# Performance work log

Measured on AMD Instinct MI355X. Metric: run time of the kernel, lower is better.

The kernel has to match this reference:

```python
import jax, jax.numpy as jnp
import numpy as np

DIM = 256
N_EMBED = 20
KL_WEIGHT = 1e-08
TAU = 1.0
EPS = 1e-10
N_RES = 3


def conv3x3(x, w, b):
    # x: [B,C,H,W], w: [O,I,3,3], b: [O]
    y = jax.lax.conv_general_dilated(
        x, w, window_strides=(1, 1), padding=((1, 1), (1, 1)),
        dimension_numbers=('NCHW', 'OIHW', 'NCHW'))
    return y + b[None, :, None, None]


def setup_inputs() -> dict:
    key = jax.random.key(0)
    ks = jax.random.split(key, 12)
    B, H, W = 8, 128, 128
    s = 1.0 / np.sqrt(DIM * 9)
    return {
        'x': jax.random.normal(ks[0], (B, DIM, H, W), dtype=jnp.float32),
        'gumbel_u': jax.random.uniform(ks[1], (B, N_EMBED, 1, 1), dtype=jnp.float32),
        'W_map': jax.random.normal(ks[2], (DIM, DIM), dtype=jnp.float32) / np.sqrt(DIM),
        'proj_w': jax.random.normal(ks[3], (N_EMBED, DIM), dtype=jnp.float32) / np.sqrt(DIM),
        'proj_b': jnp.zeros((N_EMBED,), dtype=jnp.float32),
        'embed': jax.random.normal(ks[4], (N_EMBED, DIM), dtype=jnp.float32),
        'res_w1': jax.random.normal(ks[5], (N_RES, DIM, DIM, 3, 3), dtype=jnp.float32) * s,
        'res_b1': jnp.zeros((N_RES, DIM), dtype=jnp.float32),
        'res_w2': jax.random.normal(ks[6], (N_RES, DIM, DIM, 3, 3), dtype=jnp.float32) * s,
        'res_b2': jnp.zeros((N_RES, DIM), dtype=jnp.float32),
    }


def reference(x, gumbel_u, W_map, proj_w, proj_b, embed, res_w1, res_b1, res_w2, res_b2):
    # --- mapping network: global avg pool -> 1x1 conv -> sigmoid ---
    pooled = jnp.mean(x, axis=(2, 3), keepdims=True)            # [B,C,1,1]
    m = jax.nn.sigmoid(jnp.einsum('oc,bchw->bohw', W_map, pooled))

    # --- GumbelQuantize ---
    logits = jnp.einsum('nc,bchw->bnhw', proj_w, m) + proj_b[None, :, None, None]
    g = -jnp.log(-jnp.log(gumbel_u + EPS) + EPS)                 # gumbel noise
    y_soft = jax.nn.softmax((logits + g) / TAU, axis=1)
    idx = jnp.argmax(y_soft, axis=1)                             # [B,1,1]
    y_hard = jax.nn.one_hot(idx, N_EMBED, axis=1, dtype=y_soft.dtype)
    # straight-through hard one-hot
    one_hot = y_hard + y_soft - jax.lax.stop_gradient(y_soft)
    piror = jnp.einsum('bnhw,nd->bdhw', one_hot, embed)          # [B,C,1,1]

    # KL to uniform (computed but discarded by WPGM.forward; kept for fidelity)
    qy = jax.nn.softmax(logits, axis=1)
    _diff = KL_WEIGHT * jnp.mean(jnp.sum(qy * jnp.log(qy * N_EMBED + EPS), axis=1))

    # --- residual add + 3 ResBlocks (conv3x3 -> relu -> conv3x3 + skip) ---
    h = x + piror
    for i in range(N_RES):
        h = h + conv3x3(jax.nn.relu(conv3x3(h, res_w1[i], res_b1[i])), res_w2[i], res_b2[i])
    return h
```

## Files before the change

### kernel.cpp

```cpp
#include <hip/hip_runtime.h>

typedef unsigned int uint32;
typedef __attribute__((ext_vector_type(8))) short short8;
typedef __attribute__((ext_vector_type(4))) float f32x4;

__device__ inline float bf2f(unsigned short u){ return __uint_as_float(((uint32)u)<<16); }
__device__ inline unsigned short f2bf(float f){
    uint32 x = __float_as_uint(f);
    x += 0x7fffu + ((x>>16)&1u);
    return (unsigned short)(x>>16);
}

__global__ __launch_bounds__(256) void pool_kernel(const float* __restrict__ x,
                                                   float* __restrict__ pooled){
    int bc = blockIdx.x;
    const float4* row = (const float4*)(x + (size_t)bc*16384);
    float s = 0.f;
#pragma unroll
    for(int k=0;k<16;k++){ float4 v = row[threadIdx.x + k*256]; s += v.x+v.y+v.z+v.w; }
    for(int off=32; off; off>>=1) s += __shfl_down(s, off, 64);
    __shared__ float ls[4];
    int lane = threadIdx.x & 63, w = threadIdx.x >> 6;
    if(lane==0) ls[w] = s;
    __syncthreads();
    if(threadIdx.x==0) pooled[bc] = (ls[0]+ls[1]+ls[2]+ls[3]) * (1.0f/16384.0f);
}

__global__ __launch_bounds__(256) void head_kernel(const float* __restrict__ W_map,
                                                   const float* __restrict__ proj_w,
                                                   const float* __restrict__ proj_b,
                                                   const float* __restrict__ embed,
                                                   const float* __restrict__ gu,
                                                   const float* __restrict__ pooled,
                                                   float* __restrict__ piror){
    __shared__ float m[256];
    __shared__ float lg[20];
    __shared__ int sidx;
    int t = threadIdx.x;
    for(int b=0;b<8;b++){
        float s = 0.f;
        const float* wr = W_map + (size_t)t*256;
        const float* pb = pooled + b*256;
        for(int c=0;c<256;c++) s += wr[c]*pb[c];
        m[t] = 1.0f/(1.0f+__expf(-s));
        __syncthreads();
        if(t<20){
            float s2 = 0.f;
            const float* pw = proj_w + (size_t)t*256;
            for(int c=0;c<256;c++) s2 += pw[c]*m[c];
            float u = gu[b*20+t];
            float g = -logf(-logf(u + 1e-10f) + 1e-10f);
            lg[t] = s2 + proj_b[t] + g;
        }
        __syncthreads();
        if(t==0){
            int best = 0; float bv = lg[0];
            for(int n=1;n<20;n++) if(lg[n] > bv){ bv = lg[n]; best = n; }
            sidx = best;
        }
        __syncthreads();
        piror[b*256+t] = embed[(size_t)sidx*256 + t];
        __syncthreads();
    }
}

__global__ __launch_bounds__(256) void pack_kernel(const float* __restrict__ x,
                                                   const float* __restrict__ piror,
                                                   unsigned short* __restrict__ h){
    __shared__ float tile[64][65];
    int bx = blockIdx.x;
    int b    =  bx >> 10;
    int cblk = (bx >> 8) & 3;
    int pblk =  bx & 255;
    int c0 = cblk*64, p0 = pblk*64;
    int col = threadIdx.x & 63;
    int r0  = threadIdx.x >> 6;
    const float* xb = x + ((size_t)(b*256 + c0))*16384 + p0;
#pragma unroll
    for(int it=0; it<16; it++){
        int r = r0 + it*4;
        tile[r][col] = xb[(size_t)r*16384 + col];
    }
    __syncthreads();
    float pir = piror[b*256 + c0 + col];
    unsigned short* hb = h + ((size_t)(b*16384 + p0))*256 + c0;
#pragma unroll
    for(int it=0; it<16; it++){
        int p = r0 + it*4;
        hb[(size_t)p*256 + col] = f2bf(tile[col][p] + pir);
    }
}

__global__ __launch_bounds__(256) void wtrans_kernel(const float* __restrict__ w1,
                                                     const float* __restrict__ w2,
                                                     unsigned short* __restrict__ wT){
    int bx = blockIdx.x;
    int o  = bx & 255;
    int tt = bx >> 8;
    int cv = tt / 9, tap = tt % 9;
    int res = cv >> 1;
    const float* src = ((cv & 1) ? w2 : w1) + (size_t)res * 589824;
    int c = threadIdx.x;
    float v = src[((size_t)o*256 + c)*9 + tap];
    wT[(size_t)bx*256 + c] = f2bf(v);
}

template<int MODE>
__global__ __launch_bounds__(256, 2)
void conv_kernel(const unsigned short* __restrict__ src,
                 const unsigned short* __restrict__ wTc,
                 const float* __restrict__ bias,
                 unsigned short* __restrict__ dst,
                 const unsigned short* __restrict__ hskip,
                 float* __restrict__ out,
                 const unsigned short* __restrict__ zp){
    __shared__ unsigned short ldsX[3*4160];
    __shared__ unsigned short ldsW[2][256*32];
    int tid  = threadIdx.x;
    int bid  = blockIdx.x;
    int b    = bid & 7;
    int y    = bid >> 3;
    int pt   = b*128 + y;

    int lane = tid & 63, wid = tid >> 6;
    int l15  = lane & 15, quad = lane >> 4;

    if(tid < 96){
        int r = tid >> 5, side = (tid >> 4) & 1, dw = tid & 15;
        ((int*)ldsX)[r*2080 + (side ? 129*16 : 0) + dw] = 0;
    }

    const unsigned short* xbase[6];
    int xdst[6];
#pragma unroll
    for(int t=0;t<6;t++){
        int qb = t*256 + wid*64;
        int rb = qb >> 9;
        int cb = qb & 511;
        int q  = qb + lane;
        int p  = (q & 511) >> 2;
        int k  = q & 3;
        int kk = k ^ ((p+1)&3);
        int yy = y + rb - 1;
        xbase[t] = ((unsigned)yy < 128u)
                 ? src + ((size_t)((b*128+yy)*128 + p))*256 + kk*8
                 : zp + kk*8;
        xdst[t] = rb*4160 + 32 + cb*8;
    }
    const unsigned short* wbase[4];
    int wdst[4];
#pragma unroll
    for(int t=0;t<4;t++){
        int qb = t*256 + wid*64;
        int q  = qb + lane;
        int o  = q >> 2;
        int kk = (q & 3) ^ (o & 3);
        wbase[t] = wTc + ((size_t)o)*256 + kk*8;
        wdst[t]  = qb*8;
    }
    int aoff[4];
#pragma unroll
    for(int i=0;i<4;i++){
        int o = wid*64 + i*16 + l15;
        aoff[i] = o*32 + ((quad ^ (o&3))*8);
    }

    f32x4 acc[4][8];
#pragma unroll
    for(int i=0;i<4;i++)
#pragma unroll
        for(int j=0;j<8;j++){ f32x4 z = {0.f,0.f,0.f,0.f}; acc[i][j] = z; }

    for(int cc=0; cc<8; cc++){
#pragma unroll
        for(int t=0;t<6;t++)
            __builtin_amdgcn_global_load_lds(
                (const __attribute__((address_space(1))) void*)(xbase[t] + cc*32),
                (__attribute__((address_space(3))) void*)&ldsX[xdst[t]], 16, 0, 0);
#pragma unroll
        for(int t=0;t<4;t++)
            __builtin_amdgcn_global_load_lds(
                (const __attribute__((address_space(1))) void*)(wbase[t] + cc*32),
                (__attribute__((address_space(3))) void*)&ldsW[0][wdst[t]], 16, 0, 0);
        __syncthreads();

        for(int tap=0; tap<9; tap++){
            int d = tap & 1;
            if(tap < 8){
#pragma unroll
                for(int t=0;t<4;t++)
                    __builtin_amdgcn_global_load_lds(
                        (const __attribute__((address_space(1))) void*)(wbase[t] + (size_t)(tap+1)*65536 + cc*32),
                        (__attribute__((address_space(3))) void*)&ldsW[d^1][wdst[t]], 16, 0, 0);
            }
            int rr = tap / 3;
            int dx = tap % 3 - 1;

            short8 av[4], bv[8];
#pragma unroll
            for(int i=0;i<4;i++) av[i] = *(const short8*)&ldsW[d][aoff[i]];
#pragma unroll
            for(int j=0;j<8;j++){
                int s = j*16 + l15 + dx + 1;
                bv[j] = *(const short8*)&ldsX[rr*4160 + s*32 + ((quad ^ (s&3))*8)];
            }
#pragma unroll
            for(int i=0;i<4;i++)
#pragma unroll
                for(int j=0;j<8;j++)
                    acc[i][j] = __builtin_amdgcn_mfma_f32_16x16x32_bf16(av[i], bv[j], acc[i][j], 0,0,0);
            __syncthreads();
        }
    }

    size_t gprow = (size_t)pt*128;
#pragma unroll
    for(int i=0;i<4;i++){
        int o = wid*64 + i*16 + quad*4;
        float4 bb = *(const float4*)&bias[o];
        float bias4[4] = {bb.x, bb.y, bb.z, bb.w};
#pragma unroll
        for(int j=0;j<8;j++){
            int p = j*16 + l15;
            size_t gpix = gprow + p;
            float v[4];
#pragma unroll
            for(int r=0;r<4;r++) v[r] = acc[i][j][r] + bias4[r];
            if(MODE==0){
#pragma unroll
                for(int r=0;r<4;r++) v[r] = fmaxf(v[r], 0.0f);
                ushort4 st; st.x=f2bf(v[0]); st.y=f2bf(v[1]); st.z=f2bf(v[2]); st.w=f2bf(v[3]);
                *(ushort4*)&dst[gpix*256 + o] = st;
            } else {
                ushort4 sk = *(const ushort4*)&hskip[gpix*256 + o];
                v[0]+=bf2f(sk.x); v[1]+=bf2f(sk.y); v[2]+=bf2f(sk.z); v[3]+=bf2f(sk.w);
                if(MODE==1){
                    ushort4 st; st.x=f2bf(v[0]); st.y=f2bf(v[1]); st.z=f2bf(v[2]); st.w=f2bf(v[3]);
                    *(ushort4*)&dst[gpix*256 + o] = st;
                } else {
                    size_t outbase = ((size_t)(b*256 + o))*16384 + (size_t)y*128 + p;
#pragma unroll
                    for(int r=0;r<4;r++) out[outbase + (size_t)r*16384] = v[r];
                }
            }
        }
    }
}

extern "C" void kernel_launch(void* const* d_in, const int* in_sizes, int n_in,
                              void* d_out, int out_size, void* d_ws, size_t ws_size,
                              hipStream_t stream){
    const float* x      = (const float*)d_in[0];
    const float* gu     = (const float*)d_in[1];
    const float* W_map  = (const float*)d_in[2];
    const float* proj_w = (const float*)d_in[3];
    const float* proj_b = (const float*)d_in[4];
    const float* embed  = (const float*)d_in[5];
    const float* rw1    = (const float*)d_in[6];
    const float* rb1    = (const float*)d_in[7];
    const float* rw2    = (const float*)d_in[8];
    const float* rb2    = (const float*)d_in[9];
    float* out = (float*)d_out;

    char* ws = (char*)d_ws;
    unsigned short* zp     = (unsigned short*)(ws + 0);
    float*          pooled = (float*)(ws + 4096);
    float*          piror  = (float*)(ws + 16384);
    unsigned short* wT     = (unsigned short*)(ws + 32768);
    unsigned short* hbuf   = (unsigned short*)(ws + ((size_t)8<<20));
    unsigned short* tbuf   = (unsigned short*)(ws + ((size_t)8<<20) + ((size_t)64<<20));

    hipMemsetAsync(zp, 0, 1024, stream);
    pool_kernel<<<2048, 256, 0, stream>>>(x, pooled);
    head_kernel<<<1, 256, 0, stream>>>(W_map, proj_w, proj_b, embed, gu, pooled, piror);
    pack_kernel<<<8192, 256, 0, stream>>>(x, piror, hbuf);
    wtrans_kernel<<<13824, 256, 0, stream>>>(rw1, rw2, wT);

    for(int res=0; res<3; res++){
        const unsigned short* w1c = wT + (size_t)(res*2+0)*9*65536;
        const unsigned short* w2c = wT + (size_t)(res*2+1)*9*65536;
        conv_kernel<0><<<1024, 256, 0, stream>>>(hbuf, w1c, rb1 + res*256, tbuf, nullptr, nullptr, zp);
        if(res < 2)
            conv_kernel<1><<<1024, 256, 0, stream>>>(tbuf, w2c, rb2 + res*256, hbuf, hbuf, nullptr, zp);
        else
            conv_kernel<2><<<1024, 256, 0, stream>>>(tbuf, w2c, rb2 + res*256, nullptr, hbuf, out, zp);
    }
}
```

Measured before the change: 1.241 ms.

## Load conv weights directly into registers and double-buffer input rows in LDS

Weight fragments are now read straight from global memory into registers, prefetched one tap ahead, and the LDS weight staging buffer is removed. The input-row tile becomes double-buffered, so the next channel chunk loads during compute, and the per-tap barriers are replaced by a single barrier per chunk. The LDS swizzle for the input tile changes to a pair-based XOR pattern. This trades LDS traffic and synchronisation for more global/L2 weight reads, since every wave fetches its own weight fragments, and for higher register pressure.

```diff
diff --git a/kernel.cpp b/kernel.cpp
--- a/kernel.cpp
+++ b/kernel.cpp
@@ -114,8 +114,7 @@
                  const unsigned short* __restrict__ hskip,
                  float* __restrict__ out,
                  const unsigned short* __restrict__ zp){
-    __shared__ unsigned short ldsX[3*4160];
-    __shared__ unsigned short ldsW[2][256*32];
+    __shared__ unsigned short ldsX[2][3*4160];
     int tid  = threadIdx.x;
     int bid  = blockIdx.x;
     int b    = bid & 7;
@@ -125,9 +124,9 @@
     int lane = tid & 63, wid = tid >> 6;
     int l15  = lane & 15, quad = lane >> 4;
 
-    if(tid < 96){
-        int r = tid >> 5, side = (tid >> 4) & 1, dw = tid & 15;
-        ((int*)ldsX)[r*2080 + (side ? 129*16 : 0) + dw] = 0;
+    if(tid < 192){
+        int buf = tid / 96, r = (tid % 96) >> 5, side = (tid >> 4) & 1, dw = tid & 15;
+        ((int*)ldsX)[buf*6240 + r*2080 + (side ? 2064 : 0) + dw] = 0;
     }
 
     const unsigned short* xbase[6];
@@ -140,29 +139,19 @@
         int q  = qb + lane;
         int p  = (q & 511) >> 2;
         int k  = q & 3;
-        int kk = k ^ ((p+1)&3);
+        int kk = k ^ (((p+1) >> 1) & 3);
         int yy = y + rb - 1;
         xbase[t] = ((unsigned)yy < 128u)
                  ? src + ((size_t)((b*128+yy)*128 + p))*256 + kk*8
                  : zp + kk*8;
         xdst[t] = rb*4160 + 32 + cb*8;
     }
-    const unsigned short* wbase[4];
-    int wdst[4];
-#pragma unroll
-    for(int t=0;t<4;t++){
-        int qb = t*256 + wid*64;
-        int q  = qb + lane;
-        int o  = q >> 2;
-        int kk = (q & 3) ^ (o & 3);
-        wbase[t] = wTc + ((size_t)o)*256 + kk*8;
-        wdst[t]  = qb*8;
-    }
-    int aoff[4];
+
+    const unsigned short* wfrag[4];
 #pragma unroll
     for(int i=0;i<4;i++){
         int o = wid*64 + i*16 + l15;
-        aoff[i] = o*32 + ((quad ^ (o&3))*8);
+        wfrag[i] = wTc + (size_t)o*256 + quad*8;
     }
 
     f32x4 acc[4][8];
@@ -171,46 +160,49 @@
 #pragma unroll
         for(int j=0;j<8;j++){ f32x4 z = {0.f,0.f,0.f,0.f}; acc[i][j] = z; }
 
+#pragma unroll
+    for(int t=0;t<6;t++)
+        __builtin_amdgcn_global_load_lds(
+            (const __attribute__((address_space(1))) void*)xbase[t],
+            (__attribute__((address_space(3))) void*)&ldsX[0][xdst[t]], 16, 0, 0);
+    __syncthreads();
+
     for(int cc=0; cc<8; cc++){
-#pragma unroll
-        for(int t=0;t<6;t++)
-            __builtin_amdgcn_global_load_lds(
-                (const __attribute__((address_space(1))) void*)(xbase[t] + cc*32),
-                (__attribute__((address_space(3))) void*)&ldsX[xdst[t]], 16, 0, 0);
-#pragma unroll
-        for(int t=0;t<4;t++)
-            __builtin_amdgcn_global_load_lds(
-                (const __attribute__((address_space(1))) void*)(wbase[t] + cc*32),
-                (__attribute__((address_space(3))) void*)&ldsW[0][wdst[t]], 16, 0, 0);
-        __syncthreads();
-
+        const int buf = cc & 1;
+        unsigned short* xb = &ldsX[buf][0];
+        if(cc < 7){
+#pragma unroll
+            for(int t=0;t<6;t++)
+                __builtin_amdgcn_global_load_lds(
+                    (const __attribute__((address_space(1))) void*)(xbase[t] + (cc+1)*32),
+                    (__attribute__((address_space(3))) void*)&ldsX[buf^1][xdst[t]], 16, 0, 0);
+        }
+        short8 wr[2][4];
+#pragma unroll
+        for(int i=0;i<4;i++) wr[0][i] = *(const short8*)(wfrag[i] + cc*32);
+
+#pragma unroll
         for(int tap=0; tap<9; tap++){
-            int d = tap & 1;
             if(tap < 8){
 #pragma unroll
-                for(int t=0;t<4;t++)
-                    __builtin_amdgcn_global_load_lds(
-                        (const __attribute__((address_space(1))) void*)(wbase[t] + (size_t)(tap+1)*65536 + cc*32),
-                        (__attribute__((address_space(3))) void*)&ldsW[d^1][wdst[t]], 16, 0, 0);
+                for(int i=0;i<4;i++)
+                    wr[(tap+1)&1][i] = *(const short8*)(wfrag[i] + (size_t)(tap+1)*65536 + cc*32);
             }
             int rr = tap / 3;
             int dx = tap % 3 - 1;
-
-            short8 av[4], bv[8];
-#pragma unroll
-            for(int i=0;i<4;i++) av[i] = *(const short8*)&ldsW[d][aoff[i]];
+            short8 bv[8];
 #pragma unroll
             for(int j=0;j<8;j++){
                 int s = j*16 + l15 + dx + 1;
-                bv[j] = *(const short8*)&ldsX[rr*4160 + s*32 + ((quad ^ (s&3))*8)];
+                bv[j] = *(const short8*)&xb[rr*4160 + s*32 + ((quad ^ ((s>>1)&3))*8)];
             }
 #pragma unroll
             for(int i=0;i<4;i++)
 #pragma unroll
                 for(int j=0;j<8;j++)
-                    acc[i][j] = __builtin_amdgcn_mfma_f32_16x16x32_bf16(av[i], bv[j], acc[i][j], 0,0,0);
-            __syncthreads();
-        }
+                    acc[i][j] = __builtin_amdgcn_mfma_f32_16x16x32_bf16(wr[tap&1][i], bv[j], acc[i][j], 0,0,0);
+        }
+        __syncthreads();
     }
 
     size_t gprow = (size_t)pt*128;
```

Result: slower. 1.397 ms (+12.6%).
